# Kernel tuning notes

Hardware: AMD Instinct MI355X
Metric: run time of the kernel (lower is better)

Reference implementation:

```python
import jax, jax.numpy as jnp
import numpy as np

B, S, H, R, G, L, A = 1024, 512, 2048, 64, 16, 4, 256
ADAPT_SCALE = 0.1


def setup_inputs() -> dict:
    key = jax.random.key(0)
    ks = jax.random.split(key, 12)
    w = lambda k, shp: (jax.random.normal(k, shp, dtype=jnp.float32) * 0.02)
    return {
        "s": jax.random.normal(ks[0], (B, S), dtype=jnp.float32),
        "W_in": w(ks[1], (S, H)),
        "b_in": jnp.zeros((H,), jnp.float32),
        "W_main": w(ks[2], (L, H, H)),
        "b_main": jnp.zeros((L, H), jnp.float32),
        "Wa": w(ks[3], (L, G, H, R)),   # down-projection per layer/group
        "ba": jnp.zeros((L, G, R), jnp.float32),
        "Wb": w(ks[4], (L, G, R, H)),   # up-projection per layer/group
        "bb": jnp.zeros((L, G, H), jnp.float32),
        "W_out": w(ks[5], (H, A)),
        "b_out": jnp.zeros((A,), jnp.float32),
    }


def reference(s, W_in, b_in, W_main, b_main, Wa, ba, Wb, bb, W_out, b_out):
    # g=None path: expand state across groups, then input layer (group-invariant)
    x = s @ W_in + b_in                              # [B, H]
    x = jnp.broadcast_to(x[:, None, :], (B, G, H))   # [B, G, H]
    for i in range(L):
        h = jnp.einsum("bgh,hk->bgk", x, W_main[i]) + b_main[i]          # shared main GEMM
        z = jnp.einsum("bgh,ghr->bgr", x, Wa[i]) + ba[i]                  # grouped low-rank down
        z = jnp.einsum("bgr,grh->bgh", z, Wb[i]) + bb[i]                  # grouped low-rank up
        h = h + ADAPT_SCALE * z
        x = jax.nn.elu(h)                            # dropout in eval mode = identity
    logits = jnp.einsum("bgh,ha->bga", x, W_out) + b_out  # Categorical(logits=...)
    return logits
```

## Files before the change

kernel.cpp:

```cpp
#include <hip/hip_runtime.h>
#include <cstdint>
#include <cmath>

typedef _Float16 f16;
typedef _Float16 f16x2 __attribute__((ext_vector_type(2)));
typedef _Float16 f16x4 __attribute__((ext_vector_type(4)));
typedef _Float16 f16x8 __attribute__((ext_vector_type(8)));
typedef float f32x4 __attribute__((ext_vector_type(4)));

#define DEVI static __device__ __forceinline__

constexpr int B_ = 1024, S_ = 512, H_ = 2048, R_ = 64, G_ = 16, L_ = 4, A_ = 256;
constexpr float ADAPT = 0.1f;

DEVI void gl_lds16(const void* g, void* l) {
  __builtin_amdgcn_global_load_lds((const __attribute__((address_space(1))) void*)g,
                                   (__attribute__((address_space(3))) void*)l,
                                   16, 0, 0);
}

template <int N> DEVI void wvc() {
  if constexpr (N == 0)       asm volatile("s_waitcnt vmcnt(0)");
  else if constexpr (N == 1)  asm volatile("s_waitcnt vmcnt(1)");
  else if constexpr (N == 2)  asm volatile("s_waitcnt vmcnt(2)");
  else if constexpr (N == 3)  asm volatile("s_waitcnt vmcnt(3)");
  else if constexpr (N == 4)  asm volatile("s_waitcnt vmcnt(4)");
  else if constexpr (N == 6)  asm volatile("s_waitcnt vmcnt(6)");
  else if constexpr (N == 8)  asm volatile("s_waitcnt vmcnt(8)");
  else if constexpr (N == 9)  asm volatile("s_waitcnt vmcnt(9)");
  else if constexpr (N == 12) asm volatile("s_waitcnt vmcnt(12)");
  else static_assert(N == 0, "unsupported vmcnt literal");
}

DEVI void tr64(float (*tile)[33], const float* __restrict__ src, f16* __restrict__ dst,
               int rows, int cols, float scale, int bid) {
  const int nx = cols / 32, ny = rows / 64;
  const int z = bid / (nx * ny), rem = bid % (nx * ny);
  const int cy = rem / nx, cx = rem % nx;
  src += (size_t)z * rows * cols;
  dst += (size_t)z * rows * cols;
  const int tx = threadIdx.x, ty = threadIdx.y;
  const int r0 = cy * 64, c0 = cx * 32;
  #pragma unroll
  for (int i = ty; i < 64; i += 8)
    tile[i][tx] = src[(size_t)(r0 + i) * cols + (c0 + tx)];
  __syncthreads();
  #pragma unroll
  for (int j = ty; j < 32; j += 8) {
    f16x2 v;
    v.x = (f16)(tile[2 * tx][j] * scale);
    v.y = (f16)(tile[2 * tx + 1][j] * scale);
    *(f16x2*)&dst[(size_t)(c0 + j) * rows + r0 + 2 * tx] = v;
  }
}

__global__ void prep_kernel(const float* __restrict__ s, f16* __restrict__ sh,
                            const float* __restrict__ W_in, f16* __restrict__ Wint,
                            const float* __restrict__ W_main, f16* __restrict__ Wmt,
                            const float* __restrict__ Wa, f16* __restrict__ Wat,
                            const float* __restrict__ Wb, f16* __restrict__ Wbt,
                            const float* __restrict__ W_out, f16* __restrict__ Wot) {
  __shared__ float tile[64][33];
  int bid = blockIdx.x;
  if (bid < 512) {
    int i = (bid * 256 + threadIdx.y * 32 + threadIdx.x) * 4;
    float4 v = *(const float4*)&s[i];
    f16x4 o;
    o.x = (f16)v.x; o.y = (f16)v.y; o.z = (f16)v.z; o.w = (f16)v.w;
    *(f16x4*)&sh[i] = o;
    return;
  }
  bid -= 512;
  if (bid < 512)  { tr64(tile, W_in,   Wint, S_, H_, 1.f,   bid); return; }
  bid -= 512;
  if (bid < 8192) { tr64(tile, W_main, Wmt,  H_, H_, 1.f,   bid); return; }
  bid -= 8192;
  if (bid < 4096) { tr64(tile, Wa,     Wat,  H_, R_, 1.f,   bid); return; }
  bid -= 4096;
  if (bid < 4096) { tr64(tile, Wb,     Wbt,  R_, H_, ADAPT, bid); return; }
  bid -= 4096;
  tr64(tile, W_out, Wot, H_, A_, 1.f, bid);
}

#define MQ(QM, QN, AF, BF)                                                   \
  _Pragma("unroll") for (int i = 0; i < 4; ++i)                              \
  _Pragma("unroll") for (int j = 0; j < 2; ++j)                              \
  _Pragma("unroll") for (int k = 0; k < 2; ++k)                              \
    acc[QM][QN][i][j] = __builtin_amdgcn_mfma_f32_16x16x32_f16(              \
        AF[i][k], BF[j][k], acc[QM][QN][i][j], 0, 0, 0)

#define STGM(BASE, OFF, DST) do {                                            \
    gl_lds16(BASE + OFF, &lds[DST]);                                         \
    gl_lds16(BASE + OFF + 32768, &lds[DST + 1024]);                          \
    OFF += 128; DST ^= 65536; } while (0)
#define STGC(BASE, OFF, DST) do {                                            \
    gl_lds16(BASE + OFF, &lds[DST]);                                         \
    gl_lds16(BASE + OFF + 1024, &lds[DST + 1024]);                           \
    DST ^= 65536; } while (0)
#define NOSTG ((void)0)
#define WV4 asm volatile("s_waitcnt vmcnt(4)")
#define WV0 asm volatile("s_waitcnt vmcnt(0)")
#define NOW ((void)0)
#define BAR() __builtin_amdgcn_s_barrier()
#define PRI1 __builtin_amdgcn_s_setprio(1)
#define PRI0 __builtin_amdgcn_s_setprio(0)

#define TILE3(PC, S1a, S1b, S2a, S2b, BW) do {                               \
    f16x8 a0[4][2], a1[4][2], b0[2][2], b1v[2][2];                           \
    _Pragma("unroll") for (int i = 0; i < 4; ++i) {                          \
      a0[i][0] = *(const f16x8*)&lds[(PC) + cab + i * 2048 + lof0];          \
      a0[i][1] = *(const f16x8*)&lds[(PC) + cab + i * 2048 + lof1]; }        \
    _Pragma("unroll") for (int j = 0; j < 2; ++j) {                          \
      b0[j][0] = *(const f16x8*)&lds[(PC) + cbb + j * 2048 + lof0];          \
      b0[j][1] = *(const f16x8*)&lds[(PC) + cbb + j * 2048 + lof1]; }        \
    S1a; S1b; BAR();                                                         \
    PRI1; MQ(0, 0, a0, b0); PRI0; BAR();                                     \
    _Pragma("unroll") for (int j = 0; j < 2; ++j) {                          \
      b1v[j][0] = *(const f16x8*)&lds[(PC) + cbb + 16384 + j * 2048 + lof0]; \
      b1v[j][1] = *(const f16x8*)&lds[(PC) + cbb + 16384 + j * 2048 + lof1]; } \
    S2a; S2b; BAR();                                                         \
    PRI1; MQ(0, 1, a0, b1v); PRI0; BAR();                                    \
    _Pragma("unroll") for (int i = 0; i < 4; ++i) {                          \
      a1[i][0] = *(const f16x8*)&lds[(PC) + cab + 16384 + i * 2048 + lof0];  \
      a1[i][1] = *(const f16x8*)&lds[(PC) + cab + 16384 + i * 2048 + lof1]; } \
    BAR();                                                                   \
    PRI1; MQ(1, 1, a1, b1v); MQ(1, 0, a1, b0); PRI0;                         \
    BW; BAR();                                                               \
  } while (0)

__global__ __launch_bounds__(512, 2)
void gemm8_main_kernel(const f16* __restrict__ Aacts,
                      const f16* __restrict__ Wm,
                      const f16* __restrict__ Z1,
                      const f16* __restrict__ Wb2,
                      const float* __restrict__ b1,
                      const float* __restrict__ b2,
                      f16* __restrict__ Out) {
  __shared__ __align__(16) char lds[131072];
  const int tid = threadIdx.x, lane = tid & 63, wid = tid >> 6;
  const int x = blockIdx.x & 7, local = blockIdx.x >> 3;
  const int bm0 = (x * 8 + (local & 7)) * 256, bn0 = (local >> 3) * 256;
  const int g = bm0 >> 10;
  const char* GA = (const char*)Aacts;
  const char* GB = (const char*)Wm;
  const char* GZ = (const char*)Z1;
  const char* GW2 = (const char*)(Wb2 + (size_t)g * H_ * R_);
  const float* b2g = b2 + (size_t)g * H_;

  const int srow8 = lane >> 3;
  const int scolb = ((lane & 7) ^ srow8) * 16;
  const int fr = lane & 15, fq = lane >> 4;
  const uint32_t lof0 = fr * 128 + ((fq * 16) ^ ((fr & 7) << 4));
  const uint32_t lof1 = lof0 ^ 64;

  const uint32_t rA0 = bm0 + wid * 16 + srow8;
  const uint32_t rB0 = bn0 + wid * 16 + srow8;
  uint32_t oA0 = rA0 * 4096 + scolb;
  uint32_t oA1 = oA0 + 128 * 4096;
  uint32_t oB0 = rB0 * 4096 + scolb;
  uint32_t oB1 = oB0 + 128 * 4096;
  uint32_t dA0 = wid * 2048;
  uint32_t dA1 = 16384 + wid * 2048;
  uint32_t dB0 = 32768 + wid * 2048;
  uint32_t dB1 = 49152 + wid * 2048;
  const uint32_t cab = (wid >> 2) * 8192;
  const uint32_t cbb = 32768 + (wid & 3) * 4096;

  f32x4 acc[2][2][4][2] = {};

  STGM(GA, oA0, dA0);
  STGM(GB, oB0, dB0);
  STGM(GA, oA1, dA1);
  STGM(GB, oB1, dB1);
  STGM(GA, oA0, dA0);
  STGM(GB, oB0, dB0);
  WV4;
  BAR();

  uint32_t oA0c = rA0 * 128 + scolb;
  uint32_t oA1c = oA0c + 128 * 128;
  uint32_t oB0c = rB0 * 128 + scolb;
  uint32_t oB1c = oB0c + 128 * 128;

  #pragma unroll 1
  for (int it = 0; it < 15; ++it) {
    TILE3(0,
          STGM(GB, oB1, dB1), STGM(GA, oA1, dA1),
          STGM(GA, oA0, dA0), STGM(GB, oB0, dB0), WV4);
    TILE3(65536,
          STGM(GB, oB1, dB1), STGM(GA, oA1, dA1),
          STGM(GA, oA0, dA0), STGM(GB, oB0, dB0), WV4);
  }
  TILE3(0,
        STGM(GB, oB1, dB1), STGM(GA, oA1, dA1),
        STGC(GZ, oA0c, dA0), STGC(GW2, oB0c, dB0), WV4);
  TILE3(65536,
        STGC(GW2, oB1c, dB1), STGC(GZ, oA1c, dA1),
        NOSTG, NOSTG, WV0);
  TILE3(0, NOSTG, NOSTG, NOSTG, NOSTG, NOW);

  #pragma unroll
  for (int Qn = 0; Qn < 2; ++Qn) {
    #pragma unroll
    for (int j = 0; j < 2; ++j) {
      const int col = bn0 + Qn * 128 + (wid & 3) * 32 + j * 16 + fr;
      const float bb1 = b1[col];
      const float bb2 = ADAPT * b2g[col];
      #pragma unroll
      for (int Qm = 0; Qm < 2; ++Qm)
        #pragma unroll
        for (int i = 0; i < 4; ++i)
          #pragma unroll
          for (int r = 0; r < 4; ++r) {
            const int row = bm0 + Qm * 128 + (wid >> 2) * 64 + i * 16 + fq * 4 + r;
            float v = acc[Qm][Qn][i][j][r] + bb1 + bb2;
            v = v > 0.f ? v : expm1f(v);
            Out[(size_t)row * H_ + col] = (f16)v;
          }
    }
  }
}

enum { EPI_Z1 = 0, EPI_OUT = 1, EPI_L0 = 2 };

template <int BM, int BN, int WM, int WN, int EPI>
__global__ __launch_bounds__((BM / WM) * (BN / WN) * 64)
void gemm_db_kernel(const f16* __restrict__ A, long long lda, long long Az,
                    const f16* __restrict__ Bw, long long ldb, long long Bz,
                    long long Bg, int NT,
                    const float* __restrict__ bias1, long long b1z,
                    const float* __restrict__ bias2, long long b2z,
                    const f16* __restrict__ addmat,
                    void* __restrict__ outp, long long out_z, long long ldo,
                    int rows_per_group) {
  constexpr int NW = (BM / WM) * (BN / WN);
  constexpr int FM = WM / 16, FN = WN / 16;
  constexpr int RA = BM / (NW * 16), RB = BN / (NW * 16);
  constexpr int LPT = RA + RB;
  const int tid = threadIdx.x, lane = tid & 63, wid = tid >> 6;
  const int bm0 = blockIdx.x * BM, bn0 = blockIdx.y * BN;
  const int z = blockIdx.z;
  const int gidx = (rows_per_group > 0) ? (bm0 / rows_per_group) : 0;

  __shared__ __align__(16) f16 As[4][BM * 32];
  __shared__ __align__(16) f16 Bs[4][BN * 32];

  const int wm0 = (wid / (BN / WN)) * WM;
  const int wn0 = (wid % (BN / WN)) * WN;
  const int srow = wid * 16 + (lane >> 2);
  const int scol = (lane & 3) * 8;
  const int fr = lane & 15, fq = lane >> 4;

  const f16* pa = A + (long long)z * Az + (long long)(bm0 + srow) * lda + scol;
  const f16* pb = Bw + (long long)z * Bz + (long long)gidx * Bg +
                  (long long)(bn0 + srow) * ldb + scol;
  const long long stA = (long long)(NW * 16) * lda;
  const long long stB = (long long)(NW * 16) * ldb;

  f32x4 acc[FM][FN] = {};

  auto stage = [&](int t) {
    const f16* qa = pa + t * 32;
    const f16* qb = pb + t * 32;
    const int b = t & 3;
    #pragma unroll
    for (int r = 0; r < RA; ++r)
      gl_lds16(qa + r * stA, &As[b][(r * NW + wid) * 512]);
    #pragma unroll
    for (int r = 0; r < RB; ++r)
      gl_lds16(qb + r * stB, &Bs[b][(r * NW + wid) * 512]);
  };
  auto comp = [&](int t) {
    const int b = t & 3;
    f16x8 af[FM], bf[FN];
    #pragma unroll
    for (int i = 0; i < FM; ++i)
      af[i] = *(const f16x8*)&As[b][(wm0 + i * 16 + fr) * 32 + fq * 8];
    #pragma unroll
    for (int j = 0; j < FN; ++j)
      bf[j] = *(const f16x8*)&Bs[b][(wn0 + j * 16 + fr) * 32 + fq * 8];
    #pragma unroll
    for (int i = 0; i < FM; ++i)
      #pragma unroll
      for (int j = 0; j < FN; ++j)
        acc[i][j] = __builtin_amdgcn_mfma_f32_16x16x32_f16(af[i], bf[j], acc[i][j], 0, 0, 0);
  };

  if (NT <= 4) {
    for (int t = 0; t < NT; ++t) stage(t);
    wvc<0>();
    BAR();
    for (int t = 0; t < NT; ++t) comp(t);
  } else {
    stage(0); stage(1); stage(2); stage(3);
    int t = 0;
    #pragma unroll 1
    for (; t < NT - 4; ++t) {
      wvc<3 * LPT>();
      BAR();
      comp(t);
      BAR();
      stage(t + 4);
    }
    wvc<3 * LPT>(); BAR(); comp(t); BAR(); ++t;
    wvc<2 * LPT>(); BAR(); comp(t); BAR(); ++t;
    wvc<1 * LPT>(); BAR(); comp(t); BAR(); ++t;
    wvc<0>();       BAR(); comp(t);
  }

  const float* b1p = bias1 ? bias1 + (long long)z * b1z : nullptr;
  const float* b2p = bias2 ? bias2 + (long long)gidx * b2z : nullptr;
  #pragma unroll
  for (int i = 0; i < FM; ++i) {
    #pragma unroll
    for (int j = 0; j < FN; ++j) {
      const int col = bn0 + wn0 + j * 16 + fr;
      const float b1 = b1p ? b1p[col] : 0.f;
      const float b2v = b2p ? ADAPT * b2p[col] : 0.f;
      #pragma unroll
      for (int r = 0; r < 4; ++r) {
        const int row = bm0 + wm0 + i * 16 + fq * 4 + r;
        float v = acc[i][j][r] + b1 + b2v;
        if constexpr (EPI == EPI_L0) {
          v += (float)addmat[(long long)(row & (B_ - 1)) * H_ + col];
          v = v > 0.f ? v : expm1f(v);
          ((f16*)outp)[(long long)row * ldo + col] = (f16)v;
        } else if constexpr (EPI == EPI_Z1) {
          ((f16*)outp)[(long long)z * out_z + (long long)row * ldo + col] = (f16)v;
        } else {
          const int g = row >> 10, b = row & 1023;
          ((float*)outp)[((long long)b * G_ + g) * A_ + col] = v;
        }
      }
    }
  }
}

extern "C" void kernel_launch(void* const* d_in, const int* in_sizes, int n_in,
                              void* d_out, int out_size, void* d_ws, size_t ws_size,
                              hipStream_t stream) {
  const float* s      = (const float*)d_in[0];
  const float* W_in   = (const float*)d_in[1];
  const float* b_in   = (const float*)d_in[2];
  const float* W_main = (const float*)d_in[3];
  const float* b_main = (const float*)d_in[4];
  const float* Wa     = (const float*)d_in[5];
  const float* ba     = (const float*)d_in[6];
  const float* Wb     = (const float*)d_in[7];
  const float* bb     = (const float*)d_in[8];
  const float* W_out  = (const float*)d_in[9];
  const float* b_out  = (const float*)d_in[10];

  char* ws = (char*)d_ws;
  size_t off = 0;
  auto alloc = [&](size_t bytes) -> void* {
    void* p = ws + off;
    off += (bytes + 255) & ~(size_t)255;
    return p;
  };
  f16* sh   = (f16*)alloc((size_t)B_ * S_ * 2);
  f16* Wint = (f16*)alloc((size_t)H_ * S_ * 2);
  f16* Wmt  = (f16*)alloc((size_t)L_ * H_ * H_ * 2);
  f16* Wat  = (f16*)alloc((size_t)L_ * G_ * R_ * H_ * 2);
  f16* Wbt  = (f16*)alloc((size_t)L_ * G_ * H_ * R_ * 2);
  f16* Wot  = (f16*)alloc((size_t)A_ * H_ * 2);
  f16* xh0  = (f16*)alloc((size_t)G_ * B_ * H_ * 2);
  f16* xh1  = (f16*)alloc((size_t)G_ * B_ * H_ * 2);
  f16* z1h  = (f16*)alloc((size_t)G_ * B_ * R_ * 2);
  f16* x0h  = xh1;
  f16* y0h  = xh1 + (size_t)B_ * H_;

  prep_kernel<<<17664, dim3(32, 8), 0, stream>>>(
      s, sh, W_in, Wint, W_main, Wmt, Wa, Wat, Wb, Wbt, W_out, Wot);

  gemm_db_kernel<32, 64, 32, 32, EPI_Z1><<<dim3(B_ / 32, H_ / 64, 1), 128, 0, stream>>>(
      sh, S_, 0, Wint, S_, 0, 0, S_ / 32,
      b_in, 0, nullptr, 0, nullptr, x0h, 0, H_, 0);

  gemm_db_kernel<32, 64, 32, 32, EPI_Z1><<<dim3(B_ / 32, H_ / 64, 1), 128, 0, stream>>>(
      x0h, H_, 0, Wmt, H_, 0, 0, H_ / 32,
      b_main, 0, nullptr, 0, nullptr, y0h, 0, H_, 0);

  gemm_db_kernel<32, 64, 32, 32, EPI_Z1><<<dim3(B_ / 32, 1, G_), 128, 0, stream>>>(
      x0h, H_, 0, Wat, H_, (long long)R_ * H_, 0, H_ / 32,
      ba, R_, nullptr, 0, nullptr, z1h, (long long)B_ * R_, R_, 0);

  gemm_db_kernel<64, 128, 32, 64, EPI_L0><<<dim3(G_ * B_ / 64, H_ / 128, 1), 256, 0, stream>>>(
      z1h, R_, 0, Wbt, R_, 0, (long long)H_ * R_, R_ / 32,
      nullptr, 0, bb, H_, y0h, xh0, 0, H_, B_);

  f16* cur = xh0;
  f16* nxt = xh1;
  for (int l = 1; l < L_; ++l) {
    gemm_db_kernel<32, 64, 32, 32, EPI_Z1><<<dim3(B_ / 32, 1, G_), 128, 0, stream>>>(
        cur, H_, (long long)B_ * H_,
        Wat + (size_t)l * G_ * R_ * H_, H_, (long long)R_ * H_, 0, H_ / 32,
        ba + (size_t)l * G_ * R_, R_, nullptr, 0, nullptr,
        z1h, (long long)B_ * R_, R_, 0);
    gemm8_main_kernel<<<512, 512, 0, stream>>>(
        cur, Wmt + (size_t)l * H_ * H_, z1h, Wbt + (size_t)l * G_ * H_ * R_,
        b_main + (size_t)l * H_, bb + (size_t)l * G_ * H_, nxt);
    f16* t = cur; cur = nxt; nxt = t;
  }

  gemm_db_kernel<64, 128, 32, 64, EPI_OUT><<<dim3(G_ * B_ / 64, A_ / 128, 1), 256, 0, stream>>>(
      cur, H_, 0, Wot, H_, 0, 0, H_ / 32,
      b_out, 0, nullptr, 0, nullptr, d_out, 0, A_, 0);
}
```

Measured before the change: 698.2 us.

## Add single-barrier main GEMM variant and use it for layers one and three

Adds a second main-GEMM kernel whose tile step keeps one barrier per tile instead of four. It also prefetches a single tile ahead into the other LDS buffer and waits for all outstanding loads at the end of each tile. The aim is to cut barrier stalls between the MFMA phases. The trade-off is a shallower prefetch, so global-load latency may be exposed more than in the deeper three-stage pipeline. Layer 2 still uses the original kernel, which looks like a side-by-side comparison of the two schedules.

```diff
diff --git a/kernel.cpp b/kernel.cpp
--- a/kernel.cpp
+++ b/kernel.cpp
@@ -104,6 +104,59 @@
 #define BAR() __builtin_amdgcn_s_barrier()
 #define PRI1 __builtin_amdgcn_s_setprio(1)
 #define PRI0 __builtin_amdgcn_s_setprio(0)
+
+#define MAIN_ADDR                                                            \
+  __shared__ __align__(16) char lds[131072];                                 \
+  const int tid = threadIdx.x, lane = tid & 63, wid = tid >> 6;              \
+  const int x = blockIdx.x & 7, local = blockIdx.x >> 3;                     \
+  const int bm0 = (x * 8 + (local & 7)) * 256, bn0 = (local >> 3) * 256;     \
+  const int g = bm0 >> 10;                                                   \
+  const char* GA = (const char*)Aacts;                                       \
+  const char* GB = (const char*)Wm;                                          \
+  const char* GZ = (const char*)Z1;                                          \
+  const char* GW2 = (const char*)(Wb2 + (size_t)g * H_ * R_);                \
+  const float* b2g = b2 + (size_t)g * H_;                                    \
+  const int srow8 = lane >> 3;                                               \
+  const int scolb = ((lane & 7) ^ srow8) * 16;                               \
+  const int fr = lane & 15, fq = lane >> 4;                                  \
+  const uint32_t lof0 = fr * 128 + ((fq * 16) ^ ((fr & 7) << 4));            \
+  const uint32_t lof1 = lof0 ^ 64;                                           \
+  const uint32_t rA0 = bm0 + wid * 16 + srow8;                               \
+  const uint32_t rB0 = bn0 + wid * 16 + srow8;                               \
+  uint32_t oA0 = rA0 * 4096 + scolb;                                         \
+  uint32_t oA1 = oA0 + 128 * 4096;                                           \
+  uint32_t oB0 = rB0 * 4096 + scolb;                                         \
+  uint32_t oB1 = oB0 + 128 * 4096;                                           \
+  uint32_t dA0 = wid * 2048;                                                 \
+  uint32_t dA1 = 16384 + wid * 2048;                                         \
+  uint32_t dB0 = 32768 + wid * 2048;                                         \
+  uint32_t dB1 = 49152 + wid * 2048;                                         \
+  const uint32_t cab = (wid >> 2) * 8192;                                    \
+  const uint32_t cbb = 32768 + (wid & 3) * 4096;                             \
+  f32x4 acc[2][2][4][2] = {};
+
+#define MAIN_EPILOGUE                                                        \
+  _Pragma("unroll")                                                          \
+  for (int Qn = 0; Qn < 2; ++Qn) {                                           \
+    _Pragma("unroll")                                                        \
+    for (int j = 0; j < 2; ++j) {                                            \
+      const int col = bn0 + Qn * 128 + (wid & 3) * 32 + j * 16 + fr;         \
+      const float bb1 = b1[col];                                             \
+      const float bb2 = ADAPT * b2g[col];                                    \
+      _Pragma("unroll")                                                      \
+      for (int Qm = 0; Qm < 2; ++Qm)                                         \
+        _Pragma("unroll")                                                    \
+        for (int i = 0; i < 4; ++i)                                          \
+          _Pragma("unroll")                                                  \
+          for (int r = 0; r < 4; ++r) {                                      \
+            const int row = bm0 + Qm * 128 + (wid >> 2) * 64 + i * 16 +      \
+                            fq * 4 + r;                                      \
+            float v = acc[Qm][Qn][i][j][r] + bb1 + bb2;                      \
+            v = v > 0.f ? v : expm1f(v);                                     \
+            Out[(size_t)row * H_ + col] = (f16)v;                            \
+          }                                                                  \
+    }                                                                        \
+  }
 
 #define TILE3(PC, S1a, S1b, S2a, S2b, BW) do {                               \
     f16x8 a0[4][2], a1[4][2], b0[2][2], b1v[2][2];                           \
@@ -129,45 +182,11 @@
   } while (0)
 
 __global__ __launch_bounds__(512, 2)
-void gemm8_main_kernel(const f16* __restrict__ Aacts,
-                      const f16* __restrict__ Wm,
-                      const f16* __restrict__ Z1,
-                      const f16* __restrict__ Wb2,
-                      const float* __restrict__ b1,
-                      const float* __restrict__ b2,
-                      f16* __restrict__ Out) {
-  __shared__ __align__(16) char lds[131072];
-  const int tid = threadIdx.x, lane = tid & 63, wid = tid >> 6;
-  const int x = blockIdx.x & 7, local = blockIdx.x >> 3;
-  const int bm0 = (x * 8 + (local & 7)) * 256, bn0 = (local >> 3) * 256;
-  const int g = bm0 >> 10;
-  const char* GA = (const char*)Aacts;
-  const char* GB = (const char*)Wm;
-  const char* GZ = (const char*)Z1;
-  const char* GW2 = (const char*)(Wb2 + (size_t)g * H_ * R_);
-  const float* b2g = b2 + (size_t)g * H_;
-
-  const int srow8 = lane >> 3;
-  const int scolb = ((lane & 7) ^ srow8) * 16;
-  const int fr = lane & 15, fq = lane >> 4;
-  const uint32_t lof0 = fr * 128 + ((fq * 16) ^ ((fr & 7) << 4));
-  const uint32_t lof1 = lof0 ^ 64;
-
-  const uint32_t rA0 = bm0 + wid * 16 + srow8;
-  const uint32_t rB0 = bn0 + wid * 16 + srow8;
-  uint32_t oA0 = rA0 * 4096 + scolb;
-  uint32_t oA1 = oA0 + 128 * 4096;
-  uint32_t oB0 = rB0 * 4096 + scolb;
-  uint32_t oB1 = oB0 + 128 * 4096;
-  uint32_t dA0 = wid * 2048;
-  uint32_t dA1 = 16384 + wid * 2048;
-  uint32_t dB0 = 32768 + wid * 2048;
-  uint32_t dB1 = 49152 + wid * 2048;
-  const uint32_t cab = (wid >> 2) * 8192;
-  const uint32_t cbb = 32768 + (wid & 3) * 4096;
-
-  f32x4 acc[2][2][4][2] = {};
-
+void gemm8_main_kernel(const f16* __restrict__ Aacts, const f16* __restrict__ Wm,
+                       const f16* __restrict__ Z1, const f16* __restrict__ Wb2,
+                       const float* __restrict__ b1, const float* __restrict__ b2,
+                       f16* __restrict__ Out) {
+  MAIN_ADDR
   STGM(GA, oA0, dA0);
   STGM(GB, oB0, dB0);
   STGM(GA, oA1, dA1);
@@ -176,12 +195,10 @@
   STGM(GB, oB0, dB0);
   WV4;
   BAR();
-
   uint32_t oA0c = rA0 * 128 + scolb;
   uint32_t oA1c = oA0c + 128 * 128;
   uint32_t oB0c = rB0 * 128 + scolb;
   uint32_t oB1c = oB0c + 128 * 128;
-
   #pragma unroll 1
   for (int it = 0; it < 15; ++it) {
     TILE3(0,
@@ -198,27 +215,64 @@
         STGC(GW2, oB1c, dB1), STGC(GZ, oA1c, dA1),
         NOSTG, NOSTG, WV0);
   TILE3(0, NOSTG, NOSTG, NOSTG, NOSTG, NOW);
-
-  #pragma unroll
-  for (int Qn = 0; Qn < 2; ++Qn) {
-    #pragma unroll
-    for (int j = 0; j < 2; ++j) {
-      const int col = bn0 + Qn * 128 + (wid & 3) * 32 + j * 16 + fr;
-      const float bb1 = b1[col];
-      const float bb2 = ADAPT * b2g[col];
-      #pragma unroll
-      for (int Qm = 0; Qm < 2; ++Qm)
-        #pragma unroll
-        for (int i = 0; i < 4; ++i)
-          #pragma unroll
-          for (int r = 0; r < 4; ++r) {
-            const int row = bm0 + Qm * 128 + (wid >> 2) * 64 + i * 16 + fq * 4 + r;
-            float v = acc[Qm][Qn][i][j][r] + bb1 + bb2;
-            v = v > 0.f ? v : expm1f(v);
-            Out[(size_t)row * H_ + col] = (f16)v;
-          }
-    }
-  }
+  MAIN_EPILOGUE
+}
+
+#define TILE1(PC, S1a, S1b, S2a, S2b, BW) do {                               \
+    f16x8 a0[4][2], a1[4][2], b0[2][2], b1v[2][2];                           \
+    _Pragma("unroll") for (int i = 0; i < 4; ++i) {                          \
+      a0[i][0] = *(const f16x8*)&lds[(PC) + cab + i * 2048 + lof0];          \
+      a0[i][1] = *(const f16x8*)&lds[(PC) + cab + i * 2048 + lof1]; }        \
+    _Pragma("unroll") for (int j = 0; j < 2; ++j) {                          \
+      b0[j][0] = *(const f16x8*)&lds[(PC) + cbb + j * 2048 + lof0];          \
+      b0[j][1] = *(const f16x8*)&lds[(PC) + cbb + j * 2048 + lof1]; }        \
+    S1a; S1b;                                                                \
+    PRI1; MQ(0, 0, a0, b0); PRI0;                                            \
+    _Pragma("unroll") for (int j = 0; j < 2; ++j) {                          \
+      b1v[j][0] = *(const f16x8*)&lds[(PC) + cbb + 16384 + j * 2048 + lof0]; \
+      b1v[j][1] = *(const f16x8*)&lds[(PC) + cbb + 16384 + j * 2048 + lof1]; } \
+    S2a; S2b;                                                                \
+    PRI1; MQ(0, 1, a0, b1v); PRI0;                                           \
+    _Pragma("unroll") for (int i = 0; i < 4; ++i) {                          \
+      a1[i][0] = *(const f16x8*)&lds[(PC) + cab + 16384 + i * 2048 + lof0];  \
+      a1[i][1] = *(const f16x8*)&lds[(PC) + cab + 16384 + i * 2048 + lof1]; } \
+    PRI1; MQ(1, 1, a1, b1v); MQ(1, 0, a1, b0); PRI0;                         \
+    BW; BAR();                                                               \
+  } while (0)
+
+__global__ __launch_bounds__(512, 2)
+void gemm1b_main_kernel(const f16* __restrict__ Aacts, const f16* __restrict__ Wm,
+                        const f16* __restrict__ Z1, const f16* __restrict__ Wb2,
+                        const float* __restrict__ b1, const float* __restrict__ b2,
+                        f16* __restrict__ Out) {
+  MAIN_ADDR
+  STGM(GA, oA0, dA0);
+  STGM(GA, oA1, dA1);
+  STGM(GB, oB0, dB0);
+  STGM(GB, oB1, dB1);
+  WV0;
+  BAR();
+  uint32_t oA0c = rA0 * 128 + scolb;
+  uint32_t oA1c = oA0c + 128 * 128;
+  uint32_t oB0c = rB0 * 128 + scolb;
+  uint32_t oB1c = oB0c + 128 * 128;
+  #pragma unroll 1
+  for (int it = 0; it < 15; ++it) {
+    TILE1(0,
+          STGM(GB, oB0, dB0), STGM(GB, oB1, dB1),
+          STGM(GA, oA0, dA0), STGM(GA, oA1, dA1), WV0);
+    TILE1(65536,
+          STGM(GB, oB0, dB0), STGM(GB, oB1, dB1),
+          STGM(GA, oA0, dA0), STGM(GA, oA1, dA1), WV0);
+  }
+  TILE1(0,
+        STGM(GB, oB0, dB0), STGM(GB, oB1, dB1),
+        STGM(GA, oA0, dA0), STGM(GA, oA1, dA1), WV0);
+  TILE1(65536,
+        STGC(GW2, oB0c, dB0), STGC(GW2, oB1c, dB1),
+        STGC(GZ, oA0c, dA0), STGC(GZ, oA1c, dA1), WV0);
+  TILE1(0, NOSTG, NOSTG, NOSTG, NOSTG, NOW);
+  MAIN_EPILOGUE
 }
 
 enum { EPI_Z1 = 0, EPI_OUT = 1, EPI_L0 = 2 };
@@ -397,9 +451,14 @@
         Wat + (size_t)l * G_ * R_ * H_, H_, (long long)R_ * H_, 0, H_ / 32,
         ba + (size_t)l * G_ * R_, R_, nullptr, 0, nullptr,
         z1h, (long long)B_ * R_, R_, 0);
-    gemm8_main_kernel<<<512, 512, 0, stream>>>(
-        cur, Wmt + (size_t)l * H_ * H_, z1h, Wbt + (size_t)l * G_ * H_ * R_,
-        b_main + (size_t)l * H_, bb + (size_t)l * G_ * H_, nxt);
+    if (l == 2)
+      gemm8_main_kernel<<<512, 512, 0, stream>>>(
+          cur, Wmt + (size_t)l * H_ * H_, z1h, Wbt + (size_t)l * G_ * H_ * R_,
+          b_main + (size_t)l * H_, bb + (size_t)l * G_ * H_, nxt);
+    else
+      gemm1b_main_kernel<<<512, 512, 0, stream>>>(
+          cur, Wmt + (size_t)l * H_ * H_, z1h, Wbt + (size_t)l * G_ * H_ * R_,
+          b_main + (size_t)l * H_, bb + (size_t)l * G_ * H_, nxt);
     f16* t = cur; cur = nxt; nxt = t;
   }
 
```

After: 712.6 us. +2.1%, slower.
